# Kernel tuning notes

Hardware: AMD Instinct MI355X
Metric: run time of the kernel (lower is better)

The kernel has to match this reference:

```python
import jax, jax.numpy as jnp
import numpy as np

EPS = 1e-8

def quaternion_normalize(q):
    # q: [..., 4] -> unit quaternion
    return q / (jnp.linalg.norm(q, axis=-1, keepdims=True) + EPS)

def quaternion_mul(q1, q2):
    # Hamilton product; q1, q2 broadcastable [..., 4]
    w1, x1, y1, z1 = q1[..., 0], q1[..., 1], q1[..., 2], q1[..., 3]
    w2, x2, y2, z2 = q2[..., 0], q2[..., 1], q2[..., 2], q2[..., 3]
    w = w1 * w2 - x1 * x2 - y1 * y2 - z1 * z2
    x = w1 * x2 + x1 * w2 + y1 * z2 - z1 * y2
    y = w1 * y2 - x1 * z2 + y1 * w2 + z1 * x2
    z = w1 * z2 + x1 * y2 - y1 * x2 + z1 * w2
    return jnp.stack([w, x, y, z], axis=-1)

def setup_inputs() -> dict:
    key = jax.random.key(0)
    ks = jax.random.split(key, 7)
    B, N, M, D = 2, 512, 512, 256
    return {
        "vision_feat": jax.random.normal(ks[0], (B, N, D), dtype=jnp.float32),
        "text_feat": jax.random.normal(ks[1], (B, M, D), dtype=jnp.float32),
        "Wv": jax.random.normal(ks[2], (D, D), dtype=jnp.float32) * (1.0 / np.sqrt(D)),
        "bv": jax.random.normal(ks[3], (D,), dtype=jnp.float32) * 0.01,
        "Wt": jax.random.normal(ks[4], (D, D), dtype=jnp.float32) * (1.0 / np.sqrt(D)),
        "bt": jax.random.normal(ks[5], (D,), dtype=jnp.float32) * 0.01,
        "h": jnp.float32(1.0),
    }

def reference(vision_feat, text_feat, Wv, bv, Wt, bt, h):
    B, N, D = vision_feat.shape
    M = text_feat.shape[1]
    heads = D // 4
    # project to spinors and normalize per-quaternion
    v_spinor = quaternion_normalize((vision_feat @ Wv.T + bv).reshape(B, N, heads, 4))
    t_spinor = quaternion_normalize((text_feat @ Wt.T + bt).reshape(B, M, heads, 4))
    # broadcast pairwise quaternion product v * conj(t): [B, N, M, heads, 4]
    v_exp = v_spinor[:, :, None]                      # [B, N, 1, heads, 4]
    t_conj = t_spinor[:, None, :] * jnp.array([1.0, -1.0, -1.0, -1.0], dtype=t_spinor.dtype)
    inner = quaternion_mul(v_exp, t_conj)             # [B, N, M, heads, 4]
    vec_norm = jnp.linalg.norm(inner[..., 1:], axis=-1)
    w = inner[..., 0]
    gamma = 2.0 * jnp.arctan2(vec_norm, w + EPS)
    interference = jnp.cos(gamma / 2.0) ** 2          # [B, N, M, heads]
    attn = jax.nn.softmax(interference.mean(axis=-1) / jnp.sqrt(jnp.float32(D)), axis=-1)  # [B, N, M]
    new_vision = jnp.matmul(attn, text_feat)                      # [B, N, D]
    new_text = jnp.matmul(attn.transpose(0, 2, 1), vision_feat)   # [B, M, D]
    out_vision = vision_feat + h * new_vision
    out_text = text_feat + h * new_text
    return (out_vision, out_text)
```

## Files before the change

kernel.cpp:

```cpp
#include <hip/hip_runtime.h>
#include <math.h>

#define EPS 1e-8f

typedef short bf16x8 __attribute__((ext_vector_type(8)));
typedef short bf16x4 __attribute__((ext_vector_type(4)));
typedef float f32x4  __attribute__((ext_vector_type(4)));

__device__ __forceinline__ short f2bf(float f) {
    union { float fv; unsigned u; } v; v.fv = f;
    unsigned r = v.u + 0x7fffu + ((v.u >> 16) & 1u);
    return (short)(r >> 16);
}
__device__ __forceinline__ float bf2f(short s) {
    union { unsigned u; float f; } v;
    v.u = ((unsigned)(unsigned short)s) << 16;
    return v.f;
}
__device__ __forceinline__ bf16x8 pack8(float4 a, float4 b) {
    bf16x8 p;
    p[0] = f2bf(a.x); p[1] = f2bf(a.y); p[2] = f2bf(a.z); p[3] = f2bf(a.w);
    p[4] = f2bf(b.x); p[5] = f2bf(b.y); p[6] = f2bf(b.z); p[7] = f2bf(b.w);
    return p;
}

__global__ __launch_bounds__(256) void proj_expand_kernel(
    const float* __restrict__ vis, const float* __restrict__ txt,
    const float* __restrict__ Wv, const float* __restrict__ bv,
    const float* __restrict__ Wt, const float* __restrict__ bt,
    short* __restrict__ expq)
{
    const int which = blockIdx.z;
    const float* X    = which == 0 ? vis : txt;
    const float* W    = which == 0 ? Wv : Wt;
    const float* bias = which == 0 ? bv : bt;
    short* Eo = expq + which * 1024 * 1024;

    const int r0 = blockIdx.x * 32;
    const int c0 = blockIdx.y * 64;
    const int t = threadIdx.x, lane = t & 63, wave = t >> 6;
    const int wr = (wave >> 1) * 16, wc = (wave & 1) * 32;
    const int mrow = lane & 15, quad = lane >> 4;

    __shared__ __align__(16) short As[32][72];
    __shared__ __align__(16) short Bs[64][72];

    f32x4 acc[2] = {};

    const int srow = t >> 3, skg = t & 7;
    for (int k0 = 0; k0 < 256; k0 += 64) {
        const float* xp = X + (r0 + srow) * 256 + k0 + 8 * skg;
        float4 xa = *(const float4*)xp, xb = *(const float4*)(xp + 4);
        const float* wp0 = W + (c0 + srow) * 256 + k0 + 8 * skg;
        const float* wp1 = W + (c0 + srow + 32) * 256 + k0 + 8 * skg;
        float4 wa0 = *(const float4*)wp0, wb0 = *(const float4*)(wp0 + 4);
        float4 wa1 = *(const float4*)wp1, wb1 = *(const float4*)(wp1 + 4);
        __syncthreads();
        *(bf16x8*)&As[srow][8 * skg]      = pack8(xa, xb);
        *(bf16x8*)&Bs[srow][8 * skg]      = pack8(wa0, wb0);
        *(bf16x8*)&Bs[srow + 32][8 * skg] = pack8(wa1, wb1);
        __syncthreads();
        #pragma unroll
        for (int kh = 0; kh < 2; ++kh) {
            bf16x8 a  = *(bf16x8*)&As[wr + mrow][32 * kh + 8 * quad];
            bf16x8 b0 = *(bf16x8*)&Bs[wc + mrow][32 * kh + 8 * quad];
            bf16x8 b1 = *(bf16x8*)&Bs[wc + 16 + mrow][32 * kh + 8 * quad];
            acc[0] = __builtin_amdgcn_mfma_f32_16x16x32_bf16(a, b0, acc[0], 0, 0, 0);
            acc[1] = __builtin_amdgcn_mfma_f32_16x16x32_bf16(a, b1, acc[1], 0, 0, 0);
        }
    }

    const int qbase = lane & ~3;
    #pragma unroll
    for (int j = 0; j < 2; ++j) {
        const int col  = c0 + wc + 16 * j + mrow;
        const float bb = bias[col];
        const int head = col >> 2;
        #pragma unroll
        for (int reg = 0; reg < 4; ++reg) {
            const int row = r0 + wr + quad * 4 + reg;
            float v = acc[j][reg] + bb;
            float s = v * v;
            s += __shfl_xor(s, 1, 64);
            s += __shfl_xor(s, 2, 64);
            float q = v * (1.f / (sqrtf(s) + EPS));
            float q0 = __shfl(q, qbase + 0, 64);
            float q1 = __shfl(q, qbase + 1, 64);
            float q2 = __shfl(q, qbase + 2, 64);
            float q3 = __shfl(q, qbase + 3, 64);
            bf16x4 p;
            p[0] = f2bf(q * q0); p[1] = f2bf(q * q1);
            p[2] = f2bf(q * q2); p[3] = f2bf(q * q3);
            *(bf16x4*)(Eo + row * 1024 + head * 16 + (col & 3) * 4) = p;
        }
    }
}

__global__ __launch_bounds__(256) void logits_kernel(
    const short* __restrict__ expq, short* __restrict__ E,
    float* __restrict__ rs)
{
    const int b  = blockIdx.z;
    const int r0 = blockIdx.x * 32;
    const int c0 = blockIdx.y * 64;
    const int t = threadIdx.x, lane = t & 63, wave = t >> 6;
    const int wr = (wave >> 1) * 16, wc = (wave & 1) * 32;
    const int mrow = lane & 15, quad = lane >> 4;

    __shared__ __align__(16) short As[32][72];
    __shared__ __align__(16) short Bs[64][72];

    const short* Abase = expq + (b * 512 + r0) * 1024;
    const short* Bbase = expq + (1024 + b * 512 + c0) * 1024;

    f32x4 acc[2] = {};
    const int srow = t >> 3, skg = t & 7;
    for (int k0 = 0; k0 < 1024; k0 += 64) {
        bf16x8 av = *(const bf16x8*)(Abase + srow * 1024 + k0 + 8 * skg);
        bf16x8 b0v = *(const bf16x8*)(Bbase + srow * 1024 + k0 + 8 * skg);
        bf16x8 b1v = *(const bf16x8*)(Bbase + (srow + 32) * 1024 + k0 + 8 * skg);
        __syncthreads();
        *(bf16x8*)&As[srow][8 * skg]      = av;
        *(bf16x8*)&Bs[srow][8 * skg]      = b0v;
        *(bf16x8*)&Bs[srow + 32][8 * skg] = b1v;
        __syncthreads();
        #pragma unroll
        for (int kh = 0; kh < 2; ++kh) {
            bf16x8 a  = *(bf16x8*)&As[wr + mrow][32 * kh + 8 * quad];
            bf16x8 b0 = *(bf16x8*)&Bs[wc + mrow][32 * kh + 8 * quad];
            bf16x8 b1 = *(bf16x8*)&Bs[wc + 16 + mrow][32 * kh + 8 * quad];
            acc[0] = __builtin_amdgcn_mfma_f32_16x16x32_bf16(a, b0, acc[0], 0, 0, 0);
            acc[1] = __builtin_amdgcn_mfma_f32_16x16x32_bf16(a, b1, acc[1], 0, 0, 0);
        }
    }

    float e[2][4];
    #pragma unroll
    for (int j = 0; j < 2; ++j)
        #pragma unroll
        for (int reg = 0; reg < 4; ++reg)
            e[j][reg] = __expf(acc[j][reg] * (1.f / 1024.f));

    #pragma unroll
    for (int j = 0; j < 2; ++j) {
        const int col = c0 + wc + 16 * j + mrow;
        #pragma unroll
        for (int reg = 0; reg < 4; ++reg) {
            const int row = r0 + wr + quad * 4 + reg;
            E[(b * 512 + row) * 512 + col] = f2bf(e[j][reg]);
        }
    }
    #pragma unroll
    for (int reg = 0; reg < 4; ++reg) {
        float p = e[0][reg] + e[1][reg];
        p += __shfl_xor(p, 1, 64);
        p += __shfl_xor(p, 2, 64);
        p += __shfl_xor(p, 4, 64);
        p += __shfl_xor(p, 8, 64);
        if (mrow == 0) {
            const int row = r0 + wr + quad * 4 + reg;
            rs[(b * 512 + row) * 16 + (c0 >> 5) + (wc >> 5)] = p;
        }
    }
}

__global__ __launch_bounds__(256) void out_kernel(
    const float* __restrict__ vis, const float* __restrict__ txt,
    const short* __restrict__ E, const float* __restrict__ rs,
    const float* __restrict__ hptr,
    float* __restrict__ outv, float* __restrict__ outt)
{
    const int z = blockIdx.z;
    const int b = z & 1, which = z >> 1;
    const int r0 = blockIdx.x * 32;
    const int c0 = blockIdx.y * 64;
    const int t = threadIdx.x, lane = t & 63, wave = t >> 6;
    const int wr = (wave >> 1) * 16, wc = (wave & 1) * 32;
    const int mrow = lane & 15, quad = lane >> 4;
    const float hv = hptr[0];

    const short* Eb   = E + b * 512 * 512;
    const float* S    = (which == 0 ? txt : vis) + b * 512 * 256;
    const float* base = (which == 0 ? vis : txt) + b * 512 * 256;
    float*       out  = (which == 0 ? outv : outt) + b * 512 * 256;

    __shared__ __align__(16) short As[32][72];
    __shared__ __align__(16) short Bs[64][72];
    __shared__ float rinv_s[512];

    #pragma unroll
    for (int u = 0; u < 2; ++u) {
        const int row = t + 256 * u;
        const float* p = rs + (b * 512 + row) * 16;
        float s = 0.f;
        #pragma unroll
        for (int i = 0; i < 16; ++i) s += p[i];
        rinv_s[row] = 1.f / s;
    }
    __syncthreads();

    f32x4 acc[2] = {};
    const int kkB = t >> 3, cg = t & 7;
    const int rowA = t >> 3, kgA = t & 7;
    const int nnA = t >> 2, mgA = t & 3;

    for (int k0 = 0; k0 < 512; k0 += 64) {
        float4 sa[2], sb[2];
        #pragma unroll
        for (int u = 0; u < 2; ++u) {
            const float* sp = S + (k0 + kkB + 32 * u) * 256 + c0 + 8 * cg;
            sa[u] = *(const float4*)sp; sb[u] = *(const float4*)(sp + 4);
        }
        bf16x8 arow;
        float af[8];
        if (which == 0) {
            arow = *(const bf16x8*)(Eb + (r0 + rowA) * 512 + k0 + 8 * kgA);
        } else {
            bf16x8 ev = *(const bf16x8*)(Eb + (k0 + nnA) * 512 + r0 + 8 * mgA);
            const float ri = rinv_s[k0 + nnA];
            #pragma unroll
            for (int c = 0; c < 8; ++c) af[c] = bf2f(ev[c]) * ri;
        }
        __syncthreads();
        if (which == 0) {
            *(bf16x8*)&As[rowA][8 * kgA] = arow;
        } else {
            #pragma unroll
            for (int c = 0; c < 8; ++c) As[8 * mgA + c][nnA] = f2bf(af[c]);
        }
        #pragma unroll
        for (int u = 0; u < 2; ++u) {
            const int kk = kkB + 32 * u;
            Bs[8 * cg + 0][kk] = f2bf(sa[u].x);
            Bs[8 * cg + 1][kk] = f2bf(sa[u].y);
            Bs[8 * cg + 2][kk] = f2bf(sa[u].z);
            Bs[8 * cg + 3][kk] = f2bf(sa[u].w);
            Bs[8 * cg + 4][kk] = f2bf(sb[u].x);
            Bs[8 * cg + 5][kk] = f2bf(sb[u].y);
            Bs[8 * cg + 6][kk] = f2bf(sb[u].z);
            Bs[8 * cg + 7][kk] = f2bf(sb[u].w);
        }
        __syncthreads();
        #pragma unroll
        for (int kh = 0; kh < 2; ++kh) {
            bf16x8 a  = *(bf16x8*)&As[wr + mrow][32 * kh + 8 * quad];
            bf16x8 b0 = *(bf16x8*)&Bs[wc + mrow][32 * kh + 8 * quad];
            bf16x8 b1 = *(bf16x8*)&Bs[wc + 16 + mrow][32 * kh + 8 * quad];
            acc[0] = __builtin_amdgcn_mfma_f32_16x16x32_bf16(a, b0, acc[0], 0, 0, 0);
            acc[1] = __builtin_amdgcn_mfma_f32_16x16x32_bf16(a, b1, acc[1], 0, 0, 0);
        }
    }

    #pragma unroll
    for (int j = 0; j < 2; ++j) {
        const int col = c0 + wc + 16 * j + mrow;
        #pragma unroll
        for (int reg = 0; reg < 4; ++reg) {
            const int row = r0 + wr + quad * 4 + reg;
            const float scale = which == 0 ? hv * rinv_s[row] : hv;
            out[row * 256 + col] = fmaf(scale, acc[j][reg], base[row * 256 + col]);
        }
    }
}

extern "C" void kernel_launch(void* const* d_in, const int* in_sizes, int n_in,
                              void* d_out, int out_size, void* d_ws, size_t ws_size,
                              hipStream_t stream)
{
    const float* vis = (const float*)d_in[0];
    const float* txt = (const float*)d_in[1];
    const float* Wv  = (const float*)d_in[2];
    const float* bv  = (const float*)d_in[3];
    const float* Wt  = (const float*)d_in[4];
    const float* bt  = (const float*)d_in[5];
    const float* h   = (const float*)d_in[6];

    float* outv = (float*)d_out;
    float* outt = (float*)d_out + 2 * 512 * 256;

    short* expq = (short*)d_ws;
    short* E    = expq + 2048 * 1024;
    float* rs   = (float*)(E + 1024 * 512);

    proj_expand_kernel<<<dim3(32, 4, 2), 256, 0, stream>>>(vis, txt, Wv, bv, Wt, bt, expq);
    logits_kernel<<<dim3(16, 8, 2), 256, 0, stream>>>(expq, E, rs);
    out_kernel<<<dim3(16, 4, 4), 256, 0, stream>>>(vis, txt, E, rs, h, outv, outt);
}
```

Baseline: 95.00 us.

## Drop LDS staging, pre-transpose operands, and split into per-wave 16x32 tiles

Each GEMM kernel now gives every wave its own 16x32 output tile and loads MFMA fragments straight from global memory, with no shared-memory staging and no block barriers. The logits kernel also writes a transposed copy of E. A new transpose_scale kernel writes bf16 transposes of text and of row-scaled vision, so out_kernel reads every operand K-contiguous and no longer transposes or converts in its inner loop. This trades an extra launch, extra workspace traffic and no intra-block data reuse for more parallel waves and a simpler inner loop.

```diff
diff --git a/kernel.cpp b/kernel.cpp
--- a/kernel.cpp
+++ b/kernel.cpp
@@ -30,55 +30,49 @@
     const float* __restrict__ Wt, const float* __restrict__ bt,
     short* __restrict__ expq)
 {
-    const int which = blockIdx.z;
-    const float* X    = which == 0 ? vis : txt;
-    const float* W    = which == 0 ? Wv : Wt;
-    const float* bias = which == 0 ? bv : bt;
+    const int t = threadIdx.x, lane = t & 63, wave = t >> 6;
+    const int w  = blockIdx.x * 4 + wave;
+    const int rt = w >> 3;
+    const int ct = w & 7;
+    const int which = rt >> 6;
+    const int r0 = (rt & 63) * 16;
+    const int c0 = ct * 32;
+    const float* X    = which ? txt : vis;
+    const float* W    = which ? Wt : Wv;
+    const float* bias = which ? bt : bv;
     short* Eo = expq + which * 1024 * 1024;
 
-    const int r0 = blockIdx.x * 32;
-    const int c0 = blockIdx.y * 64;
-    const int t = threadIdx.x, lane = t & 63, wave = t >> 6;
-    const int wr = (wave >> 1) * 16, wc = (wave & 1) * 32;
     const int mrow = lane & 15, quad = lane >> 4;
 
-    __shared__ __align__(16) short As[32][72];
-    __shared__ __align__(16) short Bs[64][72];
+    const float* Arow  = X + (r0 + mrow) * 256 + 8 * quad;
+    const float* Brow0 = W + (c0 + mrow) * 256 + 8 * quad;
+    const float* Brow1 = W + (c0 + 16 + mrow) * 256 + 8 * quad;
 
     f32x4 acc[2] = {};
-
-    const int srow = t >> 3, skg = t & 7;
-    for (int k0 = 0; k0 < 256; k0 += 64) {
-        const float* xp = X + (r0 + srow) * 256 + k0 + 8 * skg;
-        float4 xa = *(const float4*)xp, xb = *(const float4*)(xp + 4);
-        const float* wp0 = W + (c0 + srow) * 256 + k0 + 8 * skg;
-        const float* wp1 = W + (c0 + srow + 32) * 256 + k0 + 8 * skg;
-        float4 wa0 = *(const float4*)wp0, wb0 = *(const float4*)(wp0 + 4);
-        float4 wa1 = *(const float4*)wp1, wb1 = *(const float4*)(wp1 + 4);
-        __syncthreads();
-        *(bf16x8*)&As[srow][8 * skg]      = pack8(xa, xb);
-        *(bf16x8*)&Bs[srow][8 * skg]      = pack8(wa0, wb0);
-        *(bf16x8*)&Bs[srow + 32][8 * skg] = pack8(wa1, wb1);
-        __syncthreads();
-        #pragma unroll
-        for (int kh = 0; kh < 2; ++kh) {
-            bf16x8 a  = *(bf16x8*)&As[wr + mrow][32 * kh + 8 * quad];
-            bf16x8 b0 = *(bf16x8*)&Bs[wc + mrow][32 * kh + 8 * quad];
-            bf16x8 b1 = *(bf16x8*)&Bs[wc + 16 + mrow][32 * kh + 8 * quad];
-            acc[0] = __builtin_amdgcn_mfma_f32_16x16x32_bf16(a, b0, acc[0], 0, 0, 0);
-            acc[1] = __builtin_amdgcn_mfma_f32_16x16x32_bf16(a, b1, acc[1], 0, 0, 0);
-        }
+    #pragma unroll 4
+    for (int k0 = 0; k0 < 256; k0 += 32) {
+        float4 a0 = *(const float4*)(Arow + k0);
+        float4 a1 = *(const float4*)(Arow + k0 + 4);
+        float4 p0 = *(const float4*)(Brow0 + k0);
+        float4 p1 = *(const float4*)(Brow0 + k0 + 4);
+        float4 q0 = *(const float4*)(Brow1 + k0);
+        float4 q1 = *(const float4*)(Brow1 + k0 + 4);
+        bf16x8 af = pack8(a0, a1);
+        bf16x8 b0 = pack8(p0, p1);
+        bf16x8 b1 = pack8(q0, q1);
+        acc[0] = __builtin_amdgcn_mfma_f32_16x16x32_bf16(af, b0, acc[0], 0, 0, 0);
+        acc[1] = __builtin_amdgcn_mfma_f32_16x16x32_bf16(af, b1, acc[1], 0, 0, 0);
     }
 
     const int qbase = lane & ~3;
     #pragma unroll
     for (int j = 0; j < 2; ++j) {
-        const int col  = c0 + wc + 16 * j + mrow;
+        const int col  = c0 + 16 * j + mrow;
         const float bb = bias[col];
         const int head = col >> 2;
         #pragma unroll
         for (int reg = 0; reg < 4; ++reg) {
-            const int row = r0 + wr + quad * 4 + reg;
+            const int row = r0 + quad * 4 + reg;
             float v = acc[j][reg] + bb;
             float s = v * v;
             s += __shfl_xor(s, 1, 64);
@@ -98,40 +92,28 @@
 
 __global__ __launch_bounds__(256) void logits_kernel(
     const short* __restrict__ expq, short* __restrict__ E,
-    float* __restrict__ rs)
-{
-    const int b  = blockIdx.z;
-    const int r0 = blockIdx.x * 32;
-    const int c0 = blockIdx.y * 64;
+    short* __restrict__ ET, float* __restrict__ rs)
+{
     const int t = threadIdx.x, lane = t & 63, wave = t >> 6;
-    const int wr = (wave >> 1) * 16, wc = (wave & 1) * 32;
+    const int w  = blockIdx.x * 4 + wave;
+    const int b  = w >> 9;
+    const int nt = (w >> 4) & 31;
+    const int mt = w & 15;
+    const int r0 = nt * 16, c0 = mt * 32;
     const int mrow = lane & 15, quad = lane >> 4;
 
-    __shared__ __align__(16) short As[32][72];
-    __shared__ __align__(16) short Bs[64][72];
-
-    const short* Abase = expq + (b * 512 + r0) * 1024;
-    const short* Bbase = expq + (1024 + b * 512 + c0) * 1024;
+    const short* Ar  = expq + (b * 512 + r0 + mrow) * 1024 + 8 * quad;
+    const short* Br0 = expq + (1024 + b * 512 + c0 + mrow) * 1024 + 8 * quad;
+    const short* Br1 = Br0 + 16 * 1024;
 
     f32x4 acc[2] = {};
-    const int srow = t >> 3, skg = t & 7;
-    for (int k0 = 0; k0 < 1024; k0 += 64) {
-        bf16x8 av = *(const bf16x8*)(Abase + srow * 1024 + k0 + 8 * skg);
-        bf16x8 b0v = *(const bf16x8*)(Bbase + srow * 1024 + k0 + 8 * skg);
-        bf16x8 b1v = *(const bf16x8*)(Bbase + (srow + 32) * 1024 + k0 + 8 * skg);
-        __syncthreads();
-        *(bf16x8*)&As[srow][8 * skg]      = av;
-        *(bf16x8*)&Bs[srow][8 * skg]      = b0v;
-        *(bf16x8*)&Bs[srow + 32][8 * skg] = b1v;
-        __syncthreads();
-        #pragma unroll
-        for (int kh = 0; kh < 2; ++kh) {
-            bf16x8 a  = *(bf16x8*)&As[wr + mrow][32 * kh + 8 * quad];
-            bf16x8 b0 = *(bf16x8*)&Bs[wc + mrow][32 * kh + 8 * quad];
-            bf16x8 b1 = *(bf16x8*)&Bs[wc + 16 + mrow][32 * kh + 8 * quad];
-            acc[0] = __builtin_amdgcn_mfma_f32_16x16x32_bf16(a, b0, acc[0], 0, 0, 0);
-            acc[1] = __builtin_amdgcn_mfma_f32_16x16x32_bf16(a, b1, acc[1], 0, 0, 0);
-        }
+    #pragma unroll 4
+    for (int k0 = 0; k0 < 1024; k0 += 32) {
+        bf16x8 a  = *(const bf16x8*)(Ar  + k0);
+        bf16x8 b0 = *(const bf16x8*)(Br0 + k0);
+        bf16x8 b1 = *(const bf16x8*)(Br1 + k0);
+        acc[0] = __builtin_amdgcn_mfma_f32_16x16x32_bf16(a, b0, acc[0], 0, 0, 0);
+        acc[1] = __builtin_amdgcn_mfma_f32_16x16x32_bf16(a, b1, acc[1], 0, 0, 0);
     }
 
     float e[2][4];
@@ -143,12 +125,15 @@
 
     #pragma unroll
     for (int j = 0; j < 2; ++j) {
-        const int col = c0 + wc + 16 * j + mrow;
+        const int col = c0 + 16 * j + mrow;
+        bf16x4 pe;
         #pragma unroll
         for (int reg = 0; reg < 4; ++reg) {
-            const int row = r0 + wr + quad * 4 + reg;
-            E[(b * 512 + row) * 512 + col] = f2bf(e[j][reg]);
-        }
+            pe[reg] = f2bf(e[j][reg]);
+            const int row = r0 + quad * 4 + reg;
+            E[(b * 512 + row) * 512 + col] = pe[reg];
+        }
+        *(bf16x4*)(ET + (b * 512 + col) * 512 + r0 + quad * 4) = pe;
     }
     #pragma unroll
     for (int reg = 0; reg < 4; ++reg) {
@@ -158,106 +143,94 @@
         p += __shfl_xor(p, 4, 64);
         p += __shfl_xor(p, 8, 64);
         if (mrow == 0) {
-            const int row = r0 + wr + quad * 4 + reg;
-            rs[(b * 512 + row) * 16 + (c0 >> 5) + (wc >> 5)] = p;
-        }
-    }
+            const int row = r0 + quad * 4 + reg;
+            rs[(b * 512 + row) * 16 + (c0 >> 5)] = p;
+        }
+    }
+}
+
+__global__ __launch_bounds__(256) void transpose_scale_kernel(
+    const float* __restrict__ vis, const float* __restrict__ txt,
+    const float* __restrict__ rs,
+    short* __restrict__ txtT, short* __restrict__ visST,
+    float* __restrict__ rinv)
+{
+    const int bx = blockIdx.x;
+    const int mat = bx >> 6;
+    const int b   = (bx >> 5) & 1;
+    const int m0  = (bx & 31) * 16;
+    const int t   = threadIdx.x;
+
+    __shared__ float rsc[16];
+    if (mat == 1) {
+        if (t < 16) {
+            const float* p = rs + (b * 512 + m0 + t) * 16;
+            float s = 0.f;
+            #pragma unroll
+            for (int i = 0; i < 16; ++i) s += p[i];
+            const float ri = 1.f / s;
+            rsc[t] = ri;
+            rinv[b * 512 + m0 + t] = ri;
+        }
+        __syncthreads();
+    }
+
+    const float* src = (mat ? vis : txt) + (b * 512 + m0) * 256 + t;
+    short* dst = (mat ? visST : txtT) + (b * 256 + t) * 512 + m0;
+
+    bf16x8 v0, v1;
+    #pragma unroll
+    for (int i = 0; i < 8; ++i) {
+        float a = src[i * 256];
+        float c = src[(i + 8) * 256];
+        if (mat) { a *= rsc[i]; c *= rsc[i + 8]; }
+        v0[i] = f2bf(a);
+        v1[i] = f2bf(c);
+    }
+    *(bf16x8*)(dst)     = v0;
+    *(bf16x8*)(dst + 8) = v1;
 }
 
 __global__ __launch_bounds__(256) void out_kernel(
     const float* __restrict__ vis, const float* __restrict__ txt,
-    const short* __restrict__ E, const float* __restrict__ rs,
-    const float* __restrict__ hptr,
+    const short* __restrict__ E, const short* __restrict__ ET,
+    const short* __restrict__ txtT, const short* __restrict__ visST,
+    const float* __restrict__ rinv, const float* __restrict__ hptr,
     float* __restrict__ outv, float* __restrict__ outt)
 {
-    const int z = blockIdx.z;
-    const int b = z & 1, which = z >> 1;
-    const int r0 = blockIdx.x * 32;
-    const int c0 = blockIdx.y * 64;
     const int t = threadIdx.x, lane = t & 63, wave = t >> 6;
-    const int wr = (wave >> 1) * 16, wc = (wave & 1) * 32;
+    const int w     = blockIdx.x * 4 + wave;
+    const int which = w >> 9;
+    const int b     = (w >> 8) & 1;
+    const int nt    = (w >> 3) & 31;
+    const int dt    = w & 7;
+    const int r0 = nt * 16, c0 = dt * 32;
     const int mrow = lane & 15, quad = lane >> 4;
     const float hv = hptr[0];
 
-    const short* Eb   = E + b * 512 * 512;
-    const float* S    = (which == 0 ? txt : vis) + b * 512 * 256;
-    const float* base = (which == 0 ? vis : txt) + b * 512 * 256;
-    float*       out  = (which == 0 ? outv : outt) + b * 512 * 256;
-
-    __shared__ __align__(16) short As[32][72];
-    __shared__ __align__(16) short Bs[64][72];
-    __shared__ float rinv_s[512];
-
-    #pragma unroll
-    for (int u = 0; u < 2; ++u) {
-        const int row = t + 256 * u;
-        const float* p = rs + (b * 512 + row) * 16;
-        float s = 0.f;
-        #pragma unroll
-        for (int i = 0; i < 16; ++i) s += p[i];
-        rinv_s[row] = 1.f / s;
-    }
-    __syncthreads();
+    const short* Ar  = (which ? ET : E) + (b * 512 + r0 + mrow) * 512 + 8 * quad;
+    const short* Br0 = (which ? visST : txtT) + (b * 256 + c0 + mrow) * 512 + 8 * quad;
+    const short* Br1 = Br0 + 16 * 512;
+    const float* base = (which ? txt : vis) + (b * 512 + r0) * 256;
+    float*       out  = (which ? outt : outv) + (b * 512 + r0) * 256;
 
     f32x4 acc[2] = {};
-    const int kkB = t >> 3, cg = t & 7;
-    const int rowA = t >> 3, kgA = t & 7;
-    const int nnA = t >> 2, mgA = t & 3;
-
-    for (int k0 = 0; k0 < 512; k0 += 64) {
-        float4 sa[2], sb[2];
-        #pragma unroll
-        for (int u = 0; u < 2; ++u) {
-            const float* sp = S + (k0 + kkB + 32 * u) * 256 + c0 + 8 * cg;
-            sa[u] = *(const float4*)sp; sb[u] = *(const float4*)(sp + 4);
-        }
-        bf16x8 arow;
-        float af[8];
-        if (which == 0) {
-            arow = *(const bf16x8*)(Eb + (r0 + rowA) * 512 + k0 + 8 * kgA);
-        } else {
-            bf16x8 ev = *(const bf16x8*)(Eb + (k0 + nnA) * 512 + r0 + 8 * mgA);
-            const float ri = rinv_s[k0 + nnA];
-            #pragma unroll
-            for (int c = 0; c < 8; ++c) af[c] = bf2f(ev[c]) * ri;
-        }
-        __syncthreads();
-        if (which == 0) {
-            *(bf16x8*)&As[rowA][8 * kgA] = arow;
-        } else {
-            #pragma unroll
-            for (int c = 0; c < 8; ++c) As[8 * mgA + c][nnA] = f2bf(af[c]);
-        }
-        #pragma unroll
-        for (int u = 0; u < 2; ++u) {
-            const int kk = kkB + 32 * u;
-            Bs[8 * cg + 0][kk] = f2bf(sa[u].x);
-            Bs[8 * cg + 1][kk] = f2bf(sa[u].y);
-            Bs[8 * cg + 2][kk] = f2bf(sa[u].z);
-            Bs[8 * cg + 3][kk] = f2bf(sa[u].w);
-            Bs[8 * cg + 4][kk] = f2bf(sb[u].x);
-            Bs[8 * cg + 5][kk] = f2bf(sb[u].y);
-            Bs[8 * cg + 6][kk] = f2bf(sb[u].z);
-            Bs[8 * cg + 7][kk] = f2bf(sb[u].w);
-        }
-        __syncthreads();
-        #pragma unroll
-        for (int kh = 0; kh < 2; ++kh) {
-            bf16x8 a  = *(bf16x8*)&As[wr + mrow][32 * kh + 8 * quad];
-            bf16x8 b0 = *(bf16x8*)&Bs[wc + mrow][32 * kh + 8 * quad];
-            bf16x8 b1 = *(bf16x8*)&Bs[wc + 16 + mrow][32 * kh + 8 * quad];
-            acc[0] = __builtin_amdgcn_mfma_f32_16x16x32_bf16(a, b0, acc[0], 0, 0, 0);
-            acc[1] = __builtin_amdgcn_mfma_f32_16x16x32_bf16(a, b1, acc[1], 0, 0, 0);
-        }
-    }
-
-    #pragma unroll
-    for (int j = 0; j < 2; ++j) {
-        const int col = c0 + wc + 16 * j + mrow;
-        #pragma unroll
-        for (int reg = 0; reg < 4; ++reg) {
-            const int row = r0 + wr + quad * 4 + reg;
-            const float scale = which == 0 ? hv * rinv_s[row] : hv;
+    #pragma unroll 4
+    for (int k0 = 0; k0 < 512; k0 += 32) {
+        bf16x8 a  = *(const bf16x8*)(Ar  + k0);
+        bf16x8 b0 = *(const bf16x8*)(Br0 + k0);
+        bf16x8 b1 = *(const bf16x8*)(Br1 + k0);
+        acc[0] = __builtin_amdgcn_mfma_f32_16x16x32_bf16(a, b0, acc[0], 0, 0, 0);
+        acc[1] = __builtin_amdgcn_mfma_f32_16x16x32_bf16(a, b1, acc[1], 0, 0, 0);
+    }
+
+    #pragma unroll
+    for (int reg = 0; reg < 4; ++reg) {
+        const int row = quad * 4 + reg;
+        const float scale = which ? hv : hv * rinv[b * 512 + r0 + row];
+        #pragma unroll
+        for (int j = 0; j < 2; ++j) {
+            const int col = c0 + 16 * j + mrow;
             out[row * 256 + col] = fmaf(scale, acc[j][reg], base[row * 256 + col]);
         }
     }
@@ -278,11 +251,16 @@
     float* outv = (float*)d_out;
     float* outt = (float*)d_out + 2 * 512 * 256;
 
-    short* expq = (short*)d_ws;
-    short* E    = expq + 2048 * 1024;
-    float* rs   = (float*)(E + 1024 * 512);
-
-    proj_expand_kernel<<<dim3(32, 4, 2), 256, 0, stream>>>(vis, txt, Wv, bv, Wt, bt, expq);
-    logits_kernel<<<dim3(16, 8, 2), 256, 0, stream>>>(expq, E, rs);
-    out_kernel<<<dim3(16, 4, 4), 256, 0, stream>>>(vis, txt, E, rs, h, outv, outt);
-}
+    short* expq  = (short*)d_ws;
+    short* E     = expq + 2048 * 1024;
+    short* ET    = E + 1024 * 512;
+    float* rs    = (float*)(ET + 1024 * 512);
+    float* rinv  = rs + 1024 * 16;
+    short* txtT  = (short*)(rinv + 1024);
+    short* visST = txtT + 2 * 256 * 512;
+
+    proj_expand_kernel<<<dim3(256), 256, 0, stream>>>(vis, txt, Wv, bv, Wt, bt, expq);
+    logits_kernel<<<dim3(256), 256, 0, stream>>>(expq, E, ET, rs);
+    transpose_scale_kernel<<<dim3(128), 256, 0, stream>>>(vis, txt, rs, txtT, visST, rinv);
+    out_kernel<<<dim3(256), 256, 0, stream>>>(vis, txt, E, ET, txtT, visST, rinv, h, outv, outt);
+}
```

Result: slower. 103.7 us (+9.1%).
